# Optimization experiments

Measured on AMD Instinct MI355X. Metric: run time of the kernel, lower is better.

## Reference

```python
import jax, jax.numpy as jnp
import numpy as np

N, E, G = 10000, 320000, 256
IN_NODE, OUT_NODE, IN_EDGE, HID = 32, 32, 16, 64
BN_EPS = 1e-5


def setup_inputs() -> dict:
    key = jax.random.key(0)
    ks = jax.random.split(key, 8)
    return {
        "x": jax.random.normal(ks[0], (N, IN_NODE), jnp.float32),
        "edge_attr": jax.random.normal(ks[1], (E, IN_EDGE), jnp.float32),
        "edge_index": jax.random.randint(ks[2], (2, E), 0, N),
        "batch": jnp.sort(jax.random.randint(ks[3], (N,), 0, G)),
        "W1": jax.random.normal(ks[4], (IN_EDGE, HID), jnp.float32) * 0.1,
        "b1": jnp.zeros((HID,), jnp.float32),
        "gamma": jnp.ones((HID,), jnp.float32),
        "beta": jnp.zeros((HID,), jnp.float32),
        "W2": jax.random.normal(ks[5], (HID, IN_NODE * OUT_NODE), jnp.float32) * 0.05,
        "b2": jnp.zeros((IN_NODE * OUT_NODE,), jnp.float32),
        "W_root": jax.random.normal(ks[6], (IN_NODE, OUT_NODE), jnp.float32) * 0.1,
        "bias": jnp.zeros((OUT_NODE,), jnp.float32),
        "num_graphs": G,
    }


def reference(x, edge_attr, edge_index, batch, W1, b1, gamma, beta, W2, b2, W_root, bias, num_graphs):
    src, dst = edge_index[0], edge_index[1]
    # edge MLP: Linear -> BatchNorm1d (training-mode batch stats) -> ReLU -> Linear
    h = edge_attr @ W1 + b1                                   # [E, HID]
    mu = jnp.mean(h, axis=0)
    var = jnp.var(h, axis=0)
    h = (h - mu) * jax.lax.rsqrt(var + BN_EPS) * gamma + beta
    h = jax.nn.relu(h)
    w_e = (h @ W2 + b2).reshape(-1, x.shape[1], W_root.shape[1])  # [E, in, out]
    # gather source features, per-edge matmul, scatter-add to targets
    msgs = jnp.einsum('ei,eio->eo', x[src], w_e)              # [E, out]
    aggr = jax.ops.segment_sum(msgs, dst, num_segments=x.shape[0])
    out = aggr + x @ W_root + bias                            # [N, out]
    # global mean pool per graph
    pooled = jax.ops.segment_sum(out, batch, num_segments=num_graphs)
    counts = jax.ops.segment_sum(jnp.ones((x.shape[0],), x.dtype), batch, num_segments=num_graphs)
    return pooled / jnp.maximum(counts, 1.0)[:, None]
```

## Files before the change

kernel.cpp:

```cpp
#include <hip/hip_runtime.h>
#include <stdint.h>

typedef unsigned short u16;
typedef _Float16 f16x2 __attribute__((ext_vector_type(2)));
typedef _Float16 v8h  __attribute__((ext_vector_type(8)));
typedef float    v4f  __attribute__((ext_vector_type(4)));
union U32F16 { uint32_t u; f16x2 h; };
union ABFrag { uint32_t u[4]; v8h h; };

__device__ __forceinline__ float bf2f(u16 v) {
    union { uint32_t u; float f; } c; c.u = ((uint32_t)v) << 16; return c.f;
}
__device__ __forceinline__ u16 f2bf(float f) {
    union { uint32_t u; float f; } c; c.f = f;
    uint32_t u = c.u;
    return (u16)((u + 0x7FFF + ((u >> 16) & 1)) >> 16);
}
__device__ __forceinline__ float loadf(const void* p, size_t i, int isbf) {
    return isbf ? bf2f(((const u16*)p)[i]) : ((const float*)p)[i];
}
__device__ __forceinline__ int get_isbf(const void* gamma) {
    return ((const uint32_t*)gamma)[0] != 0x3F800000u;
}
#define LGKM_WAIT() __asm__ volatile("s_waitcnt lgkmcnt(0)" ::: "memory")

template<int P>
__device__ __forceinline__ void gram_acc(float (&pp)[8][16], float (&s8)[8],
                                         const float (&v)[16]) {
#pragma unroll
    for (int r = 0; r < 8; r++) {
        const int i = 2 * r + P;
        const float vi = v[i];
        s8[r] += vi;
#pragma unroll
        for (int j = i; j < 16; j++) pp[r][j] += vi * v[j];
    }
}
#define RED6(s) { s += __shfl_xor(s,1); s += __shfl_xor(s,2); s += __shfl_xor(s,4); \
                  s += __shfl_xor(s,8); s += __shfl_xor(s,16); s += __shfl_xor(s,32); }
template<int P>
__device__ __forceinline__ void gram_flush(float (&pp)[8][16], float (&s8)[8],
                                           float (*smS)[8], float (*smP)[8][16],
                                           int wid, int lane) {
#pragma unroll
    for (int r = 0; r < 8; r++) {
        float s = s8[r];
        RED6(s);
        if (lane == 0) smS[wid][r] = s;
#pragma unroll
        for (int j = 2 * r + P; j < 16; j++) {
            float q = pp[r][j];
            RED6(q);
            if (lane == 0) smP[wid][r][j] = q;
        }
    }
}

__global__ __launch_bounds__(256) void k_moments(
    const void* __restrict__ ea, const int* __restrict__ eidx,
    float* __restrict__ momP, int* __restrict__ cntn,
    const void* __restrict__ gamma, int E) {
    int isbf = get_isbf(gamma);
    int t = threadIdx.x;
    int lane = t & 63, wid = t >> 6;
    int p = wid & 1;
    int team = blockIdx.x * 2 + (wid >> 1);
    int nteam = gridDim.x * 2;
    __shared__ float smS[4][8];
    __shared__ float smP[4][8][16];

    float s8[8];
    float pp[8][16];
#pragma unroll
    for (int r = 0; r < 8; r++) {
        s8[r] = 0.f;
#pragma unroll
        for (int j = 0; j < 16; j++) pp[r][j] = 0.f;
    }

    for (int b = team * 64; b < E; b += nteam * 64) {
        int e = b + lane;
        bool valid = e < E;
        float v[16];
        if (!isbf) {
            const float* pe = (const float*)ea + (size_t)e * 16;
            float4 z = make_float4(0, 0, 0, 0);
            float4 A = valid ? *(const float4*)(pe + 0)  : z;
            float4 B = valid ? *(const float4*)(pe + 4)  : z;
            float4 C = valid ? *(const float4*)(pe + 8)  : z;
            float4 D = valid ? *(const float4*)(pe + 12) : z;
            v[0]=A.x; v[1]=A.y; v[2]=A.z; v[3]=A.w;
            v[4]=B.x; v[5]=B.y; v[6]=B.z; v[7]=B.w;
            v[8]=C.x; v[9]=C.y; v[10]=C.z; v[11]=C.w;
            v[12]=D.x; v[13]=D.y; v[14]=D.z; v[15]=D.w;
        } else {
            const u16* ph = (const u16*)ea + (size_t)e * 16;
            uint4 z = make_uint4(0, 0, 0, 0);
            uint4 U0 = valid ? *(const uint4*)(ph + 0) : z;
            uint4 U1 = valid ? *(const uint4*)(ph + 8) : z;
            const u16* h0 = (const u16*)&U0;
            const u16* h1 = (const u16*)&U1;
#pragma unroll
            for (int m = 0; m < 8; m++) { v[m] = bf2f(h0[m]); v[8 + m] = bf2f(h1[m]); }
        }
        if (p == 0) {
            if (valid) atomicAdd(&cntn[eidx[e]], 1);
            gram_acc<0>(pp, s8, v);
        } else {
            gram_acc<1>(pp, s8, v);
        }
    }
    if (p == 0) gram_flush<0>(pp, s8, smS, smP, wid, lane);
    else        gram_flush<1>(pp, s8, smS, smP, wid, lane);
    __syncthreads();
    if (t < 152) {
        float val;
        if (t < 16) {
            int i = t;
            val = smS[i & 1][i >> 1] + smS[(i & 1) + 2][i >> 1];
        } else {
            int pidx = t - 16, i2 = 0;
            while (pidx >= 16 - i2) { pidx -= 16 - i2; i2++; }
            int j = i2 + pidx;
            val = smP[i2 & 1][i2 >> 1][j] + smP[(i2 & 1) + 2][i2 >> 1][j];
        }
        momP[(size_t)blockIdx.x * 152 + t] = val;
    }
}

__global__ __launch_bounds__(256) void k_scanprep(
    const float* __restrict__ momP, int MB,
    const void* __restrict__ W1, const void* __restrict__ b1,
    const void* __restrict__ gamma, const void* __restrict__ beta,
    const int* __restrict__ cntn, int* __restrict__ offsets,
    float* __restrict__ W1eff, float* __restrict__ b1eff, int N, float invE) {
    __shared__ float M[16][16], S[16];
    __shared__ int ssum[256];
    int t = threadIdx.x;
    int isbf = get_isbf(gamma);
    float mval = 0.f;
    if (t < 152) {
#pragma unroll 4
        for (int b = 0; b < MB; b++) mval += momP[(size_t)b * 152 + t];
    }
    if (t < 16) S[t] = mval;
    if (t >= 16 && t < 152) {
        int p = t - 16, i2 = 0;
        while (p >= 16 - i2) { p -= 16 - i2; i2++; }
        M[i2][i2 + p] = mval; M[i2 + p][i2] = mval;
    }
    __syncthreads();
    if (t < 64) {
        int k = t;
        float w[16];
#pragma unroll
        for (int i = 0; i < 16; i++) w[i] = loadf(W1, (size_t)i * 64 + k, isbf);
        float s1 = 0.f;
#pragma unroll
        for (int i = 0; i < 16; i++) s1 += w[i] * S[i];
        s1 *= invE;
        float s2 = 0.f;
#pragma unroll
        for (int i = 0; i < 16; i++) {
            float r = 0.f;
#pragma unroll
            for (int j = 0; j < 16; j++) r += w[j] * M[i][j];
            s2 += w[i] * r;
        }
        s2 *= invE;
        float bk = loadf(b1, k, isbf);
        float mu = s1 + bk;
        float var = s2 - s1 * s1;
        float a = loadf(gamma, k, isbf) * rsqrtf(var + 1e-5f);
        b1eff[k] = bk * a + loadf(beta, k, isbf) - mu * a;
#pragma unroll
        for (int i = 0; i < 16; i++) W1eff[i * 64 + k] = w[i] * a;
    }
    int chunk = (N + 255) >> 8;
    int lo = min(t * chunk, N), hi = min(lo + chunk, N);
    int s = 0;
    for (int i = lo; i < hi; i++) s += cntn[i];
    ssum[t] = s; __syncthreads();
    for (int d = 1; d < 256; d <<= 1) {
        int v = (t >= d) ? ssum[t - d] : 0;
        __syncthreads();
        ssum[t] += v;
        __syncthreads();
    }
    int run = ssum[t] - s;
    for (int i = lo; i < hi; i++) { offsets[i] = run; run += cntn[i]; }
    if (t == 255) offsets[N] = run;
}

__global__ __launch_bounds__(256) void k_place(
    const int* __restrict__ eidx, const int* __restrict__ offsets,
    int* __restrict__ cursor, int2* __restrict__ eg,
    const int* __restrict__ batch, int E) {
    int e = blockIdx.x * 256 + threadIdx.x;
    if (e < E) {
        int s = eidx[e];
        int pos = offsets[s] + atomicAdd(&cursor[s], 1);
        int g = batch[eidx[E + e]];
        eg[pos] = make_int2(e, g);
    }
}

__global__ __launch_bounds__(256, 3) void k_nodeQ(
    const void* __restrict__ ea, const int2* __restrict__ eg,
    const void* __restrict__ x, const void* __restrict__ W2, const void* __restrict__ b2,
    const float* __restrict__ W1eff, const float* __restrict__ b1eff,
    const int* __restrict__ offsets, float* __restrict__ pooledA8,
    const void* __restrict__ gamma, int N, int E, int G) {
    __shared__ int offs[5];
    __shared__ float xs[4][32], Rs[4][32];
    __shared__ alignas(16) uint32_t UB[4][1056];
    int t = threadIdx.x;
    int n0 = blockIdx.x * 4;
    if (t < 5) offs[t] = offsets[min(n0 + t, N)];
    int isbf = get_isbf(gamma);
    if (t < 128) {
        int nn = t >> 5, i = t & 31;
        int n = n0 + nn;
        xs[nn][i] = (n < N) ? loadf(x, (size_t)n * 32 + i, isbf) : 0.f;
    }
    __syncthreads();
    if (offs[0] == offs[4]) return;

    {
        int o = t & 31, j2 = t >> 5;
        if (!isbf) {
            const float* W2f = (const float*)W2;
            for (int m = 0; m < 4; m++) {
                int jp = j2 + 8 * m;
                size_t base = (size_t)(2 * jp) * 1024 + o;
                float a[4][2];
#pragma unroll
                for (int nn = 0; nn < 4; nn++) { a[nn][0] = 0.f; a[nn][1] = 0.f; }
#pragma unroll 4
                for (int i = 0; i < 32; i++) {
                    float w0 = W2f[base + i * 32];
                    float w1 = W2f[base + 1024 + i * 32];
#pragma unroll
                    for (int nn = 0; nn < 4; nn++) {
                        float xv = xs[nn][i];
                        a[nn][0] += xv * w0; a[nn][1] += xv * w1;
                    }
                }
#pragma unroll
                for (int nn = 0; nn < 4; nn++) {
                    U32F16 p; p.h.x = (_Float16)a[nn][0]; p.h.y = (_Float16)a[nn][1];
                    UB[nn][jp * 33 + o] = p.u;
                }
            }
        } else {
            const u16* W2h = (const u16*)W2;
            for (int m = 0; m < 4; m++) {
                int jp = j2 + 8 * m;
                size_t base = (size_t)(2 * jp) * 1024 + o;
                float a[4][2];
#pragma unroll
                for (int nn = 0; nn < 4; nn++) { a[nn][0] = 0.f; a[nn][1] = 0.f; }
#pragma unroll 4
                for (int i = 0; i < 32; i++) {
                    float w0 = bf2f(W2h[base + i * 32]);
                    float w1 = bf2f(W2h[base + 1024 + i * 32]);
#pragma unroll
                    for (int nn = 0; nn < 4; nn++) {
                        float xv = xs[nn][i];
                        a[nn][0] += xv * w0; a[nn][1] += xv * w1;
                    }
                }
#pragma unroll
                for (int nn = 0; nn < 4; nn++) {
                    U32F16 p; p.h.x = (_Float16)a[nn][0]; p.h.y = (_Float16)a[nn][1];
                    UB[nn][jp * 33 + o] = p.u;
                }
            }
        }
    }
    if (t < 128) {
        int nn = t >> 5, o = t & 31;
        float acc = 0.f;
#pragma unroll 8
        for (int i = 0; i < 32; i++) acc += xs[nn][i] * loadf(b2, (size_t)i * 32 + o, isbf);
        Rs[nn][o] = acc;
    }
    __syncthreads();

    int w = t >> 6, lane = t & 63;
    int lo = offs[w], hi = offs[w + 1];
    int q = lane >> 4, c = lane & 15;
    int half = lane >> 5, kp = lane & 31;
    uint32_t bfr[2][2][4];
#pragma unroll
    for (int kh = 0; kh < 2; kh++)
#pragma unroll
        for (int oh = 0; oh < 2; oh++)
#pragma unroll
            for (int jj = 0; jj < 4; jj++)
                bfr[kh][oh][jj] = UB[w][(kh * 16 + q * 4 + jj) * 33 + oh * 16 + c];
    float Rv2[2] = { Rs[w][c], Rs[w][16 + c] };
    LGKM_WAIT();
    float*    eaw_w = (float*)&UB[w][0];
    uint32_t* hwb_w = &UB[w][320];
    float w1a[16], w1b[16];
#pragma unroll
    for (int i = 0; i < 16; i++) {
        w1a[i] = W1eff[i * 64 + 2 * kp];
        w1b[i] = W1eff[i * 64 + 2 * kp + 1];
    }
    float bka = b1eff[2 * kp], bkb = b1eff[2 * kp + 1];
    float* poolbase = pooledA8 + (size_t)(blockIdx.x & 7) * G * 32;

    if (lo >= hi) return;

    int2 egc = make_int2(-1, 0), egn = make_int2(-1, 0);
    { int j = lo + (lane & 15); if (lane < 16 && j < hi) egc = eg[j]; }
    { int j = lo + 16 + (lane & 15); if (lane < 16 && j < hi) egn = eg[j]; }
    float4 eaf = make_float4(0, 0, 0, 0);
    uint4  eab = make_uint4(0, 0, 0, 0);
    if (!isbf) {
        int es = __shfl(egc.x, lane >> 2);
        if (es >= 0) eaf = *(const float4*)((const float*)ea + (size_t)es * 16 + (lane & 3) * 4);
    } else {
        int es = __shfl(egc.x, lane >> 1);
        if (lane < 32 && es >= 0) eab = *(const uint4*)((const u16*)ea + (size_t)es * 16 + (lane & 1) * 8);
    }

    for (int j0 = lo; j0 < hi; j0 += 16) {
        int nvalid = min(16, hi - j0);
        if (!isbf) {
            int m = lane >> 2, qq = lane & 3;
            *(float4*)&eaw_w[m * 20 + qq * 4] = eaf;
        } else if (lane < 32) {
            int m = lane >> 1, hh = lane & 1;
            const u16* h8 = (const u16*)&eab;
            float4 f0 = make_float4(bf2f(h8[0]), bf2f(h8[1]), bf2f(h8[2]), bf2f(h8[3]));
            float4 f1 = make_float4(bf2f(h8[4]), bf2f(h8[5]), bf2f(h8[6]), bf2f(h8[7]));
            *(float4*)&eaw_w[m * 20 + hh * 8] = f0;
            *(float4*)&eaw_w[m * 20 + hh * 8 + 4] = f1;
        }
        int2 eg2 = make_int2(-1, 0);
        { int j = j0 + 32 + (lane & 15); if (lane < 16 && j < hi) eg2 = eg[j]; }
        float4 eaf_n = make_float4(0, 0, 0, 0);
        uint4  eab_n = make_uint4(0, 0, 0, 0);
        if (!isbf) {
            int es = __shfl(egn.x, lane >> 2);
            if (es >= 0) eaf_n = *(const float4*)((const float*)ea + (size_t)es * 16 + (lane & 3) * 4);
        } else {
            int es = __shfl(egn.x, lane >> 1);
            if (lane < 32 && es >= 0) eab_n = *(const uint4*)((const u16*)ea + (size_t)es * 16 + (lane & 1) * 8);
        }
        LGKM_WAIT();
#pragma unroll
        for (int m8 = 0; m8 < 8; m8++) {
            int e = half + 2 * m8;
            if (e < nvalid) {
                float ee[16];
                const float4* ep = (const float4*)&eaw_w[e * 20];
                *(float4*)&ee[0] = ep[0]; *(float4*)&ee[4] = ep[1];
                *(float4*)&ee[8] = ep[2]; *(float4*)&ee[12] = ep[3];
                float va = bka, vb = bkb;
#pragma unroll
                for (int i = 0; i < 16; i++) { va += ee[i] * w1a[i]; vb += ee[i] * w1b[i]; }
                U32F16 ph;
                ph.h.x = (_Float16)fmaxf(va, 0.f);
                ph.h.y = (_Float16)fmaxf(vb, 0.f);
                hwb_w[e * 33 + kp] = ph.u;
            }
        }
        LGKM_WAIT();
        ABFrag a0, a1;
#pragma unroll
        for (int jj = 0; jj < 4; jj++) {
            a0.u[jj] = hwb_w[c * 33 + q * 4 + jj];
            a1.u[jj] = hwb_w[c * 33 + 16 + q * 4 + jj];
        }
#pragma unroll
        for (int oh = 0; oh < 2; oh++) {
            ABFrag b0, b1f;
#pragma unroll
            for (int jj = 0; jj < 4; jj++) { b0.u[jj] = bfr[0][oh][jj]; b1f.u[jj] = bfr[1][oh][jj]; }
            v4f d = {0.f, 0.f, 0.f, 0.f};
            d = __builtin_amdgcn_mfma_f32_16x16x32_f16(a0.h, b0.h, d, 0, 0, 0);
            d = __builtin_amdgcn_mfma_f32_16x16x32_f16(a1.h, b1f.h, d, 0, 0, 0);
#pragma unroll
            for (int r = 0; r < 4; r++) {
                int e = q * 4 + r;
                int g = __shfl(egc.y, e);
                if (e < nvalid)
                    atomicAdd(poolbase + (size_t)g * 32 + oh * 16 + c, d[r] + Rv2[oh]);
            }
        }
        egc = egn; egn = eg2; eaf = eaf_n; eab = eab_n;
    }
}

__global__ __launch_bounds__(256) void k_final(
    const float* __restrict__ pooledA8, const void* __restrict__ x,
    const int* __restrict__ batch, const void* __restrict__ Wr,
    const void* __restrict__ bias, void* __restrict__ out,
    const void* __restrict__ gamma, int N, int G) {
    __shared__ float px[8][32];
    __shared__ float Sx[32];
    int g = blockIdx.x;
    int t = threadIdx.x, row = t >> 5, o = t & 31;
    int isbf = get_isbf(gamma);
    int slo = 0, shi = N;
    { int a = 0, b = N; while (a < b) { int m = (a + b) >> 1; if (batch[m] < g) a = m + 1; else b = m; } slo = a; }
    { int a = slo, b = N; while (a < b) { int m = (a + b) >> 1; if (batch[m] < g + 1) a = m + 1; else b = m; } shi = a; }
    float acc = 0.f;
    for (int n = slo + row; n < shi; n += 8) acc += loadf(x, (size_t)n * 32 + o, isbf);
    px[row][o] = acc;
    __syncthreads();
    if (t < 32) {
        float s = 0.f;
#pragma unroll
        for (int r = 0; r < 8; r++) s += px[r][t];
        Sx[t] = s;
    }
    __syncthreads();
    if (t < 32) {
        float v = 0.f;
#pragma unroll
        for (int sh = 0; sh < 8; sh++) v += pooledA8[((size_t)sh * G + g) * 32 + t];
#pragma unroll 8
        for (int i = 0; i < 32; i++) v += Sx[i] * loadf(Wr, (size_t)i * 32 + t, isbf);
        int cnt = shi - slo;
        v += (float)cnt * loadf(bias, t, isbf);
        v /= (float)max(cnt, 1);
        if (isbf) ((u16*)out)[g * 32 + t] = f2bf(v);
        else ((float*)out)[g * 32 + t] = v;
    }
}

extern "C" void kernel_launch(void* const* d_in, const int* in_sizes, int n_in,
                              void* d_out, int out_size, void* d_ws, size_t ws_size,
                              hipStream_t stream) {
    const void* x    = d_in[0];
    const void* ea   = d_in[1];
    const int* eidx  = (const int*)d_in[2];
    const int* batch = (const int*)d_in[3];
    const void* W1   = d_in[4];
    const void* b1   = d_in[5];
    const void* gamma= d_in[6];
    const void* beta = d_in[7];
    const void* W2   = d_in[8];
    const void* b2   = d_in[9];
    const void* Wr   = d_in[10];
    const void* bias = d_in[11];

    int N = in_sizes[0] / 32;
    int E = in_sizes[1] / 16;
    int G = out_size / 32;

    const int MB = 256;

    char* ws = (char*)d_ws;
    size_t off = 0;
    auto alloc = [&](size_t bytes) {
        char* p = ws + off;
        off = (off + bytes + 255) & ~(size_t)255;
        return p;
    };
    float* pooledA8 = (float*)alloc((size_t)8 * G * 32 * 4);
    int*   cntn     = (int*)alloc((size_t)N * 4);
    int*   cursor   = (int*)alloc((size_t)N * 4);
    size_t zero_bytes = off;
    float* momP     = (float*)alloc((size_t)MB * 152 * 4);
    int*   offsets  = (int*)alloc((size_t)(N + 1) * 4);
    int2*  eg       = (int2*)alloc((size_t)E * 8);
    float* W1eff    = (float*)alloc(1024 * 4);
    float* b1eff    = (float*)alloc(64 * 4);
    (void)ws_size; (void)n_in;

    hipMemsetAsync(d_ws, 0, zero_bytes, stream);
    k_moments<<<MB, 256, 0, stream>>>(ea, eidx, momP, cntn, gamma, E);
    k_scanprep<<<1, 256, 0, stream>>>(momP, MB, W1, b1, gamma, beta, cntn, offsets,
                                      W1eff, b1eff, N, 1.0f / (float)E);
    k_place<<<(E + 255) / 256, 256, 0, stream>>>(eidx, offsets, cursor, eg, batch, E);
    k_nodeQ<<<(N + 3) / 4, 256, 0, stream>>>(ea, eg, x, W2, b2, W1eff, b1eff,
                                             offsets, pooledA8, gamma, N, E, G);
    k_final<<<G, 256, 0, stream>>>(pooledA8, x, batch, Wr, bias, d_out, gamma, N, G);
}
```

Measured before the change: 276.9 us.

## Compute edge MLP first layer with MFMA instead of scalar FMAs

Replaces the per-lane scalar 16x64 first-layer matmul (BN-folded W1, ReLU) with four f16 MFMA 16x16x32 ops. Edge attributes now reach the A fragment through wave shuffles instead of being staged in LDS, with the upper K half zero-padded. The MFMA output is packed to f16 pairs with shfl_xor and written to LDS as before. Rounding edge_attr and W1 to f16 before the multiply adds precision risk. Separately, the moment-reduction block count MB drops from 256 to 64.

```diff
diff --git a/kernel.cpp b/kernel.cpp
--- a/kernel.cpp
+++ b/kernel.cpp
@@ -290,7 +290,6 @@
     int w = t >> 6, lane = t & 63;
     int lo = offs[w], hi = offs[w + 1];
     int q = lane >> 4, c = lane & 15;
-    int half = lane >> 5, kp = lane & 31;
     uint32_t bfr[2][2][4];
 #pragma unroll
     for (int kh = 0; kh < 2; kh++)
@@ -301,15 +300,25 @@
                 bfr[kh][oh][jj] = UB[w][(kh * 16 + q * 4 + jj) * 33 + oh * 16 + c];
     float Rv2[2] = { Rs[w][c], Rs[w][16 + c] };
     LGKM_WAIT();
-    float*    eaw_w = (float*)&UB[w][0];
-    uint32_t* hwb_w = &UB[w][320];
-    float w1a[16], w1b[16];
-#pragma unroll
-    for (int i = 0; i < 16; i++) {
-        w1a[i] = W1eff[i * 64 + 2 * kp];
-        w1b[i] = W1eff[i * 64 + 2 * kp + 1];
-    }
-    float bka = b1eff[2 * kp], bkb = b1eff[2 * kp + 1];
+    uint32_t* hwb_w = &UB[w][0];
+
+    ABFrag w1f[4];
+    float biasT[4];
+#pragma unroll
+    for (int T = 0; T < 4; T++) {
+        if (lane < 32) {
+#pragma unroll
+            for (int jj = 0; jj < 4; jj++) {
+                U32F16 pk;
+                pk.h.x = (_Float16)W1eff[(8 * q + 2 * jj    ) * 64 + T * 16 + c];
+                pk.h.y = (_Float16)W1eff[(8 * q + 2 * jj + 1) * 64 + T * 16 + c];
+                w1f[T].u[jj] = pk.u;
+            }
+        } else {
+            w1f[T].u[0] = 0; w1f[T].u[1] = 0; w1f[T].u[2] = 0; w1f[T].u[3] = 0;
+        }
+        biasT[T] = b1eff[T * 16 + c];
+    }
     float* poolbase = pooledA8 + (size_t)(blockIdx.x & 7) * G * 32;
 
     if (lo >= hi) return;
@@ -329,17 +338,6 @@
 
     for (int j0 = lo; j0 < hi; j0 += 16) {
         int nvalid = min(16, hi - j0);
-        if (!isbf) {
-            int m = lane >> 2, qq = lane & 3;
-            *(float4*)&eaw_w[m * 20 + qq * 4] = eaf;
-        } else if (lane < 32) {
-            int m = lane >> 1, hh = lane & 1;
-            const u16* h8 = (const u16*)&eab;
-            float4 f0 = make_float4(bf2f(h8[0]), bf2f(h8[1]), bf2f(h8[2]), bf2f(h8[3]));
-            float4 f1 = make_float4(bf2f(h8[4]), bf2f(h8[5]), bf2f(h8[6]), bf2f(h8[7]));
-            *(float4*)&eaw_w[m * 20 + hh * 8] = f0;
-            *(float4*)&eaw_w[m * 20 + hh * 8 + 4] = f1;
-        }
         int2 eg2 = make_int2(-1, 0);
         { int j = j0 + 32 + (lane & 15); if (lane < 16 && j < hi) eg2 = eg[j]; }
         float4 eaf_n = make_float4(0, 0, 0, 0);
@@ -351,22 +349,45 @@
             int es = __shfl(egn.x, lane >> 1);
             if (lane < 32 && es >= 0) eab_n = *(const uint4*)((const u16*)ea + (size_t)es * 16 + (lane & 1) * 8);
         }
-        LGKM_WAIT();
-#pragma unroll
-        for (int m8 = 0; m8 < 8; m8++) {
-            int e = half + 2 * m8;
-            if (e < nvalid) {
-                float ee[16];
-                const float4* ep = (const float4*)&eaw_w[e * 20];
-                *(float4*)&ee[0] = ep[0]; *(float4*)&ee[4] = ep[1];
-                *(float4*)&ee[8] = ep[2]; *(float4*)&ee[12] = ep[3];
-                float va = bka, vb = bkb;
-#pragma unroll
-                for (int i = 0; i < 16; i++) { va += ee[i] * w1a[i]; vb += ee[i] * w1b[i]; }
-                U32F16 ph;
-                ph.h.x = (_Float16)fmaxf(va, 0.f);
-                ph.h.y = (_Float16)fmaxf(vb, 0.f);
-                hwb_w[e * 33 + kp] = ph.u;
+        ABFrag ah;
+        if (!isbf) {
+            int sa = (c << 2) + (q << 1);
+            float p0 = __shfl(eaf.x, sa),     p1 = __shfl(eaf.y, sa);
+            float p2 = __shfl(eaf.z, sa),     p3 = __shfl(eaf.w, sa);
+            float p4 = __shfl(eaf.x, sa + 1), p5 = __shfl(eaf.y, sa + 1);
+            float p6 = __shfl(eaf.z, sa + 1), p7 = __shfl(eaf.w, sa + 1);
+            U32F16 u0, u1, u2, u3;
+            u0.h.x = (_Float16)p0; u0.h.y = (_Float16)p1;
+            u1.h.x = (_Float16)p2; u1.h.y = (_Float16)p3;
+            u2.h.x = (_Float16)p4; u2.h.y = (_Float16)p5;
+            u3.h.x = (_Float16)p6; u3.h.y = (_Float16)p7;
+            ah.u[0] = u0.u; ah.u[1] = u1.u; ah.u[2] = u2.u; ah.u[3] = u3.u;
+        } else {
+            int sa = (c << 1) + q;
+            uint32_t b0 = (uint32_t)__shfl((int)eab.x, sa);
+            uint32_t b1v = (uint32_t)__shfl((int)eab.y, sa);
+            uint32_t b2v = (uint32_t)__shfl((int)eab.z, sa);
+            uint32_t b3 = (uint32_t)__shfl((int)eab.w, sa);
+            U32F16 u0, u1, u2, u3;
+            u0.h.x = (_Float16)bf2f((u16)(b0 & 0xffff)); u0.h.y = (_Float16)bf2f((u16)(b0 >> 16));
+            u1.h.x = (_Float16)bf2f((u16)(b1v & 0xffff)); u1.h.y = (_Float16)bf2f((u16)(b1v >> 16));
+            u2.h.x = (_Float16)bf2f((u16)(b2v & 0xffff)); u2.h.y = (_Float16)bf2f((u16)(b2v >> 16));
+            u3.h.x = (_Float16)bf2f((u16)(b3 & 0xffff)); u3.h.y = (_Float16)bf2f((u16)(b3 >> 16));
+            ah.u[0] = u0.u; ah.u[1] = u1.u; ah.u[2] = u2.u; ah.u[3] = u3.u;
+        }
+        if (lane >= 32) { ah.u[0] = 0; ah.u[1] = 0; ah.u[2] = 0; ah.u[3] = 0; }
+#pragma unroll
+        for (int T = 0; T < 4; T++) {
+            v4f cb = { biasT[T], biasT[T], biasT[T], biasT[T] };
+            v4f hD = __builtin_amdgcn_mfma_f32_16x16x32_f16(ah.h, w1f[T].h, cb, 0, 0, 0);
+#pragma unroll
+            for (int r = 0; r < 4; r++) {
+                float hv = fmaxf(hD[r], 0.f);
+                float pv = __shfl_xor(hv, 1);
+                if (!(c & 1)) {
+                    U32F16 pk; pk.h.x = (_Float16)hv; pk.h.y = (_Float16)pv;
+                    hwb_w[(q * 4 + r) * 33 + T * 8 + (c >> 1)] = pk.u;
+                }
             }
         }
         LGKM_WAIT();
@@ -454,7 +475,7 @@
     int E = in_sizes[1] / 16;
     int G = out_size / 32;
 
-    const int MB = 256;
+    const int MB = 64;
 
     char* ws = (char*)d_ws;
     size_t off = 0;
```

New measurement: 312.3 us. +12.8%, slower.
